# Optimization experiments

Measured on AMD Instinct MI355X. Metric: run time of the kernel, lower is better.

The kernel has to match this reference:

```python
import jax, jax.numpy as jnp
import numpy as np

# Allpass biquad coefficients (torchaudio.functional.allpass_biquad semantics)
SAMPLE_RATE = 16000
CENTRAL_FREQ = 4000.0
Q = 0.707

def _allpass_coeffs(sample_rate, central_freq, q):
    w0 = 2.0 * np.pi * central_freq / sample_rate
    alpha = np.sin(w0) / (2.0 * q)
    cos_w0 = np.cos(w0)
    b0 = 1.0 - alpha
    b1 = -2.0 * cos_w0
    b2 = 1.0 + alpha
    a0 = 1.0 + alpha
    a1 = -2.0 * cos_w0
    a2 = 1.0 - alpha
    # normalize by a0 (as torchaudio.biquad does)
    return (np.float32(b0 / a0), np.float32(b1 / a0), np.float32(b2 / a0),
            np.float32(a1 / a0), np.float32(a2 / a0))

B0, B1, B2, A1, A2 = _allpass_coeffs(SAMPLE_RATE, CENTRAL_FREQ, Q)


def setup_inputs() -> dict:
    key = jax.random.key(0)
    x = jax.random.normal(key, (64, 1, 480000), dtype=jnp.float32)
    return {"x": x}


def _biquad(x):
    # x: [B, 1, T] -> y: [B, 1, T]
    B, C, T = x.shape
    xt = jnp.transpose(x[:, 0, :])  # [T, B] for time-major scan

    def step(carry, xn):
        x1, x2, y1, y2 = carry
        yn = B0 * xn + B1 * x1 + B2 * x2 - A1 * y1 - A2 * y2
        return (xn, x1, yn, y1), yn

    z = jnp.zeros((B,), dtype=x.dtype)
    _, yt = jax.lax.scan(step, (z, z, z, z), xt)
    return jnp.transpose(yt)[:, None, :]  # back to [B, 1, T]


def reference(x):
    return _biquad(x)
```

## Files before the change

### kernel.cpp

```cpp
#include <hip/hip_runtime.h>
#include <cmath>

#define T_LEN   480000
#define BATCH   64
#define CHUNK   16
#define WARM    16
#define TPB     256
#define TS      (TPB * CHUNK)
#define TPR     ((T_LEN + TS - 1) / TS)
#define NLOAD_MAX (TS + WARM)
#define NITER   ((NLOAD_MAX + TPB * 4 - 1) / (TPB * 4))
#define LDS_SLOTS (NLOAD_MAX + ((NLOAD_MAX >> 5) << 2))

__device__ __forceinline__ int slot4(int i) { return i + ((i >> 5) << 2); }

#define STEP(XN, YN)                                            \
    {                                                           \
        float u_ = fmaf(B0, (XN), fmaf(B1, x1, B2 * x2));       \
        (YN) = fmaf(-A1, y1, fmaf(-A2, y2, u_));                \
        x2 = x1; x1 = (XN); y2 = y1; y1 = (YN);                 \
    }

__global__ __launch_bounds__(TPB) void allpass_kernel(
    const float* __restrict__ x, float* __restrict__ y,
    float B0, float B1, float B2, float A1, float A2)
{
    __shared__ __align__(16) float lds[LDS_SLOTS];
    const int tid  = threadIdx.x;
    const int row  = blockIdx.x / TPR;
    const int tb   = blockIdx.x % TPR;
    const int sbase = tb * TS;
    const int ns   = min(TS, T_LEN - sbase);
    const float* __restrict__ xr = x + (size_t)row * T_LEN + sbase;
    float* __restrict__ yr       = y + (size_t)row * T_LEN + sbase;
    const int nload = ns + WARM;

    float4 vbuf[NITER];
    #pragma unroll
    for (int j = 0; j < NITER; ++j) {
        const int i4 = tid * 4 + j * (TPB * 4);
        if (i4 < nload) {
            if (tb == 0 && i4 < WARM)
                vbuf[j] = make_float4(0.f, 0.f, 0.f, 0.f);
            else
                vbuf[j] = *(const float4*)(xr - WARM + i4);
        }
    }
    #pragma unroll
    for (int j = 0; j < NITER; ++j) {
        const int i4 = tid * 4 + j * (TPB * 4);
        if (i4 < nload)
            *(float4*)&lds[slot4(i4)] = vbuf[j];
    }
    __syncthreads();

    const int ls = tid * CHUNK;
    if (ls < ns) {
        float x1 = 0.f, x2 = 0.f, y1 = 0.f, y2 = 0.f;
        #pragma unroll
        for (int t4 = 0; t4 < WARM; t4 += 4) {
            float4 xv = *(const float4*)&lds[slot4(ls + t4)];
            float t;
            STEP(xv.x, t); STEP(xv.y, t); STEP(xv.z, t); STEP(xv.w, t);
        }
        #pragma unroll
        for (int t4 = 0; t4 < CHUNK; t4 += 4) {
            float4 xv = *(const float4*)&lds[slot4(ls + WARM + t4)];
            float4 yv;
            STEP(xv.x, yv.x); STEP(xv.y, yv.y);
            STEP(xv.z, yv.z); STEP(xv.w, yv.w);
            *(float4*)(yr + ls + t4) = yv;
        }
    }
}

extern "C" void kernel_launch(void* const* d_in, const int* in_sizes, int n_in,
                              void* d_out, int out_size, void* d_ws, size_t ws_size,
                              hipStream_t stream) {
    const float* x = (const float*)d_in[0];
    float* y = (float*)d_out;

    const double sample_rate = 16000.0, central_freq = 4000.0, Q = 0.707;
    const double w0 = 2.0 * M_PI * central_freq / sample_rate;
    const double alpha = sin(w0) / (2.0 * Q);
    const double cw = cos(w0);
    const double a0 = 1.0 + alpha;
    const float B0 = (float)((1.0 - alpha) / a0);
    const float B1 = (float)((-2.0 * cw) / a0);
    const float B2 = (float)((1.0 + alpha) / a0);
    const float A1 = (float)((-2.0 * cw) / a0);
    const float A2 = (float)((1.0 - alpha) / a0);

    const int blocks = BATCH * TPR;
    allpass_kernel<<<blocks, TPB, 0, stream>>>(x, y, B0, B1, B2, A1, A2);
}
```

Baseline: 218.6 us.

## Process four tiles per block with register-prefetch of the next tile

Each block now handles four consecutive time tiles of a row instead of one. The load of the next tile's input is issued into registers before the current tile's recurrence is computed out of LDS, so global memory latency overlaps with compute. This cuts the block count by four and adds an extra barrier per tile, which lowers the parallelism available to hide latency across the GPU.

```diff
diff --git a/kernel.cpp b/kernel.cpp
--- a/kernel.cpp
+++ b/kernel.cpp
@@ -8,6 +8,8 @@
 #define TPB     256
 #define TS      (TPB * CHUNK)
 #define TPR     ((T_LEN + TS - 1) / TS)
+#define TPB_TILES 4
+#define BPR     ((TPR + TPB_TILES - 1) / TPB_TILES)
 #define NLOAD_MAX (TS + WARM)
 #define NITER   ((NLOAD_MAX + TPB * 4 - 1) / (TPB * 4))
 #define LDS_SLOTS (NLOAD_MAX + ((NLOAD_MAX >> 5) << 2))
@@ -27,50 +29,70 @@
 {
     __shared__ __align__(16) float lds[LDS_SLOTS];
     const int tid  = threadIdx.x;
-    const int row  = blockIdx.x / TPR;
-    const int tb   = blockIdx.x % TPR;
-    const int sbase = tb * TS;
-    const int ns   = min(TS, T_LEN - sbase);
-    const float* __restrict__ xr = x + (size_t)row * T_LEN + sbase;
-    float* __restrict__ yr       = y + (size_t)row * T_LEN + sbase;
-    const int nload = ns + WARM;
+    const int row  = blockIdx.x / BPR;
+    const int tb0  = (blockIdx.x % BPR) * TPB_TILES;
+    const int ntile = min(TPB_TILES, TPR - tb0);
+    const float* __restrict__ xrow = x + (size_t)row * T_LEN;
+    float* __restrict__ yrow       = y + (size_t)row * T_LEN;
 
+    int sbase = tb0 * TS;
+    int ns    = min(TS, T_LEN - sbase);
+    int nload = ns + WARM;
     float4 vbuf[NITER];
     #pragma unroll
     for (int j = 0; j < NITER; ++j) {
         const int i4 = tid * 4 + j * (TPB * 4);
         if (i4 < nload) {
-            if (tb == 0 && i4 < WARM)
+            if (tb0 == 0 && i4 < WARM)
                 vbuf[j] = make_float4(0.f, 0.f, 0.f, 0.f);
             else
-                vbuf[j] = *(const float4*)(xr - WARM + i4);
+                vbuf[j] = *(const float4*)(xrow + sbase - WARM + i4);
         }
     }
-    #pragma unroll
-    for (int j = 0; j < NITER; ++j) {
-        const int i4 = tid * 4 + j * (TPB * 4);
-        if (i4 < nload)
-            *(float4*)&lds[slot4(i4)] = vbuf[j];
-    }
-    __syncthreads();
 
-    const int ls = tid * CHUNK;
-    if (ls < ns) {
-        float x1 = 0.f, x2 = 0.f, y1 = 0.f, y2 = 0.f;
+    for (int it = 0; it < ntile; ++it) {
         #pragma unroll
-        for (int t4 = 0; t4 < WARM; t4 += 4) {
-            float4 xv = *(const float4*)&lds[slot4(ls + t4)];
-            float t;
-            STEP(xv.x, t); STEP(xv.y, t); STEP(xv.z, t); STEP(xv.w, t);
+        for (int j = 0; j < NITER; ++j) {
+            const int i4 = tid * 4 + j * (TPB * 4);
+            if (i4 < nload)
+                *(float4*)&lds[slot4(i4)] = vbuf[j];
         }
-        #pragma unroll
-        for (int t4 = 0; t4 < CHUNK; t4 += 4) {
-            float4 xv = *(const float4*)&lds[slot4(ls + WARM + t4)];
-            float4 yv;
-            STEP(xv.x, yv.x); STEP(xv.y, yv.y);
-            STEP(xv.z, yv.z); STEP(xv.w, yv.w);
-            *(float4*)(yr + ls + t4) = yv;
+        __syncthreads();
+
+        const int cur_sbase = sbase, cur_ns = ns;
+
+        if (it + 1 < ntile) {
+            const int tb = tb0 + it + 1;
+            sbase = tb * TS;
+            ns    = min(TS, T_LEN - sbase);
+            nload = ns + WARM;
+            #pragma unroll
+            for (int j = 0; j < NITER; ++j) {
+                const int i4 = tid * 4 + j * (TPB * 4);
+                if (i4 < nload)
+                    vbuf[j] = *(const float4*)(xrow + sbase - WARM + i4);
+            }
         }
+
+        const int ls = tid * CHUNK;
+        if (ls < cur_ns) {
+            float x1 = 0.f, x2 = 0.f, y1 = 0.f, y2 = 0.f;
+            #pragma unroll
+            for (int t4 = 0; t4 < WARM; t4 += 4) {
+                float4 xv = *(const float4*)&lds[slot4(ls + t4)];
+                float t;
+                STEP(xv.x, t); STEP(xv.y, t); STEP(xv.z, t); STEP(xv.w, t);
+            }
+            #pragma unroll
+            for (int t4 = 0; t4 < CHUNK; t4 += 4) {
+                float4 xv = *(const float4*)&lds[slot4(ls + WARM + t4)];
+                float4 yv;
+                STEP(xv.x, yv.x); STEP(xv.y, yv.y);
+                STEP(xv.z, yv.z); STEP(xv.w, yv.w);
+                *(float4*)(yrow + cur_sbase + ls + t4) = yv;
+            }
+        }
+        __syncthreads();
     }
 }
 
@@ -91,6 +113,6 @@
     const float A1 = (float)((-2.0 * cw) / a0);
     const float A2 = (float)((1.0 - alpha) / a0);
 
-    const int blocks = BATCH * TPR;
+    const int blocks = BATCH * BPR;
     allpass_kernel<<<blocks, TPB, 0, stream>>>(x, y, B0, B1, B2, A1, A2);
 }
```

Result: slower. 225.5 us (+3.1%).

## Drop LDS staging and process larger per-thread chunks directly from global memory

Applied to the files above, without the earlier changes.

Removes the shared-memory staging and block barrier. Each thread now loads its own warm-up plus a 64-sample chunk directly into registers via float4 loads and runs the recurrence. The larger chunk lowers the relative cost of redundant warm-up reads and computation. The trade-off is strided, less coalesced global access across threads and longer serial dependency chains per thread.

```diff
diff --git a/kernel.cpp b/kernel.cpp
--- a/kernel.cpp
+++ b/kernel.cpp
@@ -3,16 +3,14 @@
 
 #define T_LEN   480000
 #define BATCH   64
-#define CHUNK   16
+#define CHUNK   64
 #define WARM    16
 #define TPB     256
-#define TS      (TPB * CHUNK)
-#define TPR     ((T_LEN + TS - 1) / TS)
-#define NLOAD_MAX (TS + WARM)
-#define NITER   ((NLOAD_MAX + TPB * 4 - 1) / (TPB * 4))
-#define LDS_SLOTS (NLOAD_MAX + ((NLOAD_MAX >> 5) << 2))
+#define SEG_PER_ROW (T_LEN / CHUNK)
+#define BPR     ((SEG_PER_ROW + TPB - 1) / TPB)
+#define NV      ((WARM + CHUNK) / 4)
+#define NW      (WARM / 4)
 
-__device__ __forceinline__ int slot4(int i) { return i + ((i >> 5) << 2); }
 
 #define STEP(XN, YN)                                            \
     {                                                           \
@@ -25,52 +23,40 @@
     const float* __restrict__ x, float* __restrict__ y,
     float B0, float B1, float B2, float A1, float A2)
 {
-    __shared__ __align__(16) float lds[LDS_SLOTS];
-    const int tid  = threadIdx.x;
-    const int row  = blockIdx.x / TPR;
-    const int tb   = blockIdx.x % TPR;
-    const int sbase = tb * TS;
-    const int ns   = min(TS, T_LEN - sbase);
-    const float* __restrict__ xr = x + (size_t)row * T_LEN + sbase;
-    float* __restrict__ yr       = y + (size_t)row * T_LEN + sbase;
-    const int nload = ns + WARM;
+    const int row = blockIdx.x / BPR;
+    const int seg = (blockIdx.x % BPR) * TPB + threadIdx.x;
+    if (seg >= SEG_PER_ROW) return;
+    const size_t base = (size_t)row * T_LEN + (size_t)seg * CHUNK;
 
-    float4 vbuf[NITER];
+    float4 v[NV];
+    if (seg != 0) {
+        const float* __restrict__ xp = x + base - WARM;
+        #pragma unroll
+        for (int j = 0; j < NV; ++j)
+            v[j] = *(const float4*)(xp + 4 * j);
+    } else {
+        #pragma unroll
+        for (int j = 0; j < NW; ++j)
+            v[j] = make_float4(0.f, 0.f, 0.f, 0.f);
+        const float* __restrict__ xp = x + base;
+        #pragma unroll
+        for (int j = NW; j < NV; ++j)
+            v[j] = *(const float4*)(xp + 4 * (j - NW));
+    }
+
+    float x1 = 0.f, x2 = 0.f, y1 = 0.f, y2 = 0.f;
     #pragma unroll
-    for (int j = 0; j < NITER; ++j) {
-        const int i4 = tid * 4 + j * (TPB * 4);
-        if (i4 < nload) {
-            if (tb == 0 && i4 < WARM)
-                vbuf[j] = make_float4(0.f, 0.f, 0.f, 0.f);
-            else
-                vbuf[j] = *(const float4*)(xr - WARM + i4);
-        }
+    for (int j = 0; j < NW; ++j) {
+        float t;
+        STEP(v[j].x, t); STEP(v[j].y, t); STEP(v[j].z, t); STEP(v[j].w, t);
     }
+    float* __restrict__ yp = y + base;
     #pragma unroll
-    for (int j = 0; j < NITER; ++j) {
-        const int i4 = tid * 4 + j * (TPB * 4);
-        if (i4 < nload)
-            *(float4*)&lds[slot4(i4)] = vbuf[j];
-    }
-    __syncthreads();
-
-    const int ls = tid * CHUNK;
-    if (ls < ns) {
-        float x1 = 0.f, x2 = 0.f, y1 = 0.f, y2 = 0.f;
-        #pragma unroll
-        for (int t4 = 0; t4 < WARM; t4 += 4) {
-            float4 xv = *(const float4*)&lds[slot4(ls + t4)];
-            float t;
-            STEP(xv.x, t); STEP(xv.y, t); STEP(xv.z, t); STEP(xv.w, t);
-        }
-        #pragma unroll
-        for (int t4 = 0; t4 < CHUNK; t4 += 4) {
-            float4 xv = *(const float4*)&lds[slot4(ls + WARM + t4)];
-            float4 yv;
-            STEP(xv.x, yv.x); STEP(xv.y, yv.y);
-            STEP(xv.z, yv.z); STEP(xv.w, yv.w);
-            *(float4*)(yr + ls + t4) = yv;
-        }
+    for (int j = NW; j < NV; ++j) {
+        float4 yv;
+        STEP(v[j].x, yv.x); STEP(v[j].y, yv.y);
+        STEP(v[j].z, yv.z); STEP(v[j].w, yv.w);
+        *(float4*)(yp + 4 * (j - NW)) = yv;
     }
 }
 
@@ -91,6 +77,6 @@
     const float A1 = (float)((-2.0 * cw) / a0);
     const float A2 = (float)((1.0 - alpha) / a0);
 
-    const int blocks = BATCH * TPR;
+    const int blocks = BATCH * BPR;
     allpass_kernel<<<blocks, TPB, 0, stream>>>(x, y, B0, B1, B2, A1, A2);
 }
```

Result: slower. 260.8 us (+19.3%).
